# Kernel tuning notes

Measured on AMD Instinct MI355X. Metric: run time of the kernel, lower is better.

The kernel has to match this reference:

```python
import jax, jax.numpy as jnp
import numpy as np

B, N, D = 2, 1024, 1024
H, DH = 16, 64          # nhead, head_dim (D = H*DH)
FF = 4096               # dim_feedforward = 4*D
E = 8                   # num experts
EPS = 1e-5


def layer_norm(x, s, b):
    m = jnp.mean(x, -1, keepdims=True)
    v = jnp.mean((x - m) ** 2, -1, keepdims=True)
    return (x - m) * jax.lax.rsqrt(v + EPS) * s + b


def moe_gate(x, Wg):
    # top-1 gating: expert index + gate probability per token
    probs = jax.nn.softmax(x @ Wg, axis=-1)            # [B,N,E]
    idx = jnp.argmax(probs, axis=-1)                   # [B,N]
    gw = jnp.take_along_axis(probs, idx[..., None], -1)[..., 0]  # [B,N]
    return idx, gw


def moe_linear(x, W, b, idx, gw):
    # x:[B,N,Din], W:[E,Din,Dout], b:[E,Dout]; route each token to expert idx
    y = jnp.einsum('bnd,edh->bneh', x, W) + b          # [B,N,E,Dout]
    oh = jax.nn.one_hot(idx, E, dtype=x.dtype)         # [B,N,E]
    return jnp.einsum('bneh,bne->bnh', y, oh) * gw[..., None]


def setup_inputs() -> dict:
    key = jax.random.key(0)
    ks = jax.random.split(key, 8)
    g = lambda k, shape, sc: jax.random.normal(k, shape, jnp.float32) * sc
    inv_d = 1.0 / np.sqrt(D)
    return dict(
        src=g(ks[0], (B, N, D), 1.0),
        key_padding_mask=jnp.zeros((B, N), dtype=bool),
        Wg_attn=g(ks[1], (D, E), inv_d),
        Wqkv=g(ks[2], (E, D, 3 * D), inv_d), bqkv=jnp.zeros((E, 3 * D), jnp.float32),
        Wo=g(ks[3], (E, D, D), inv_d), bo=jnp.zeros((E, D), jnp.float32),
        Wg_ffn=g(ks[4], (D, E), inv_d),
        W1=g(ks[5], (E, D, FF), inv_d), b1=jnp.zeros((E, FF), jnp.float32),
        W2=g(ks[6], (E, FF, D), 1.0 / np.sqrt(FF)), b2=jnp.zeros((E, D), jnp.float32),
        ln1_s=jnp.ones((D,), jnp.float32), ln1_b=jnp.zeros((D,), jnp.float32),
        ln2_s=jnp.ones((D,), jnp.float32), ln2_b=jnp.zeros((D,), jnp.float32),
    )


def reference(src, key_padding_mask, Wg_attn, Wqkv, bqkv, Wo, bo,
              Wg_ffn, W1, b1, W2, b2, ln1_s, ln1_b, ln2_s, ln2_b):
    # attention mask: key_padding_mask.unsqueeze(1).unsqueeze(1) * -10000
    mask = jnp.where(key_padding_mask[:, None, None, :], -10000.0, 0.0).astype(src.dtype)

    # --- MoE self-attention (gate decided once, reused for qkv and dense) ---
    idx, gw = moe_gate(src, Wg_attn)
    qkv = moe_linear(src, Wqkv, bqkv, idx, gw)                 # [B,N,3D]
    q, k, v = jnp.split(qkv, 3, axis=-1)
    heads = lambda t: t.reshape(B, N, H, DH).transpose(0, 2, 1, 3)  # [B,H,N,DH]
    q, k, v = heads(q), heads(k), heads(v)
    scores = jnp.einsum('bhqd,bhkd->bhqk', q, k) / np.sqrt(DH) + mask
    probs = jax.nn.softmax(scores, axis=-1)
    ctx = jnp.einsum('bhqk,bhkd->bhqd', probs, v)
    ctx = ctx.transpose(0, 2, 1, 3).reshape(B, N, D)
    attn_out = moe_linear(ctx, Wo, bo, idx, gw)

    # post-norm residual
    x = layer_norm(src + attn_out, ln1_s, ln1_b)

    # --- MoE FFN (its own gate, shared across both linears) ---
    fidx, fgw = moe_gate(x, Wg_ffn)
    h = jax.nn.gelu(moe_linear(x, W1, b1, fidx, fgw))
    ffn = moe_linear(h, W2, b2, fidx, fgw)

    return layer_norm(x + ffn, ln2_s, ln2_b)
```

## Files before the change

### kernel.cpp

```cpp
#include <hip/hip_runtime.h>


#define B_   2
#define N_   1024
#define D_   1024
#define H_   16
#define DH_  64
#define FF_  4096
#define E_   8
#define NTOK 2048

typedef __attribute__((ext_vector_type(8))) short short8;
typedef __attribute__((ext_vector_type(8))) unsigned short ushort8;
typedef __attribute__((ext_vector_type(4))) unsigned short ushort4v;
typedef __attribute__((ext_vector_type(4))) float f32x4;
typedef __attribute__((ext_vector_type(2))) unsigned int uint32x2;

__device__ inline unsigned short f2bf(float f) {
  unsigned u = __float_as_uint(f);
  u += 0x7FFFu + ((u >> 16) & 1u);
  return (unsigned short)(u >> 16);
}

__device__ inline float gelu_tanh(float x) {
  float x3 = x * x * x;
  float t = tanhf(0.7978845608028654f * (x + 0.044715f * x3));
  return 0.5f * x * (1.0f + t);
}

__global__ __launch_bounds__(256) void gate_kernel(
    const float* __restrict__ X, const float* __restrict__ Wg,
    int* __restrict__ idx, float* __restrict__ gwv, int* __restrict__ cnt) {
  int t = blockIdx.x * 4 + (threadIdx.x >> 6);
  int lane = threadIdx.x & 63;
  const float* x = X + (size_t)t * D_;
  float acc[E_];
#pragma unroll
  for (int j = 0; j < E_; j++) acc[j] = 0.f;
#pragma unroll
  for (int i = 0; i < 16; i++) {
    int d = i * 64 + lane;
    float xv = x[d];
    const float4* w = (const float4*)(Wg + (size_t)d * E_);
    float4 w0 = w[0], w1 = w[1];
    acc[0] += xv * w0.x; acc[1] += xv * w0.y; acc[2] += xv * w0.z; acc[3] += xv * w0.w;
    acc[4] += xv * w1.x; acc[5] += xv * w1.y; acc[6] += xv * w1.z; acc[7] += xv * w1.w;
  }
#pragma unroll
  for (int o = 1; o < 64; o <<= 1) {
#pragma unroll
    for (int j = 0; j < E_; j++) acc[j] += __shfl_xor(acc[j], o, 64);
  }
  float m = acc[0]; int bi = 0;
#pragma unroll
  for (int j = 1; j < E_; j++) { if (acc[j] > m) { m = acc[j]; bi = j; } }
  float den = 0.f;
#pragma unroll
  for (int j = 0; j < E_; j++) den += expf(acc[j] - m);
  float gw = expf(acc[bi] - m) / den;
  if (lane == 0) { idx[t] = bi; gwv[t] = gw; atomicAdd(&cnt[bi], 1); }
}

__global__ __launch_bounds__(256) void route_kernel(
    const int* __restrict__ idx, const int* __restrict__ cnt,
    int* __restrict__ off, int* __restrict__ perm, int ntok) {
  __shared__ int loff[E_ + 1];
  __shared__ int lfill[E_];
  if (threadIdx.x == 0) {
    int s = 0;
    for (int e = 0; e < E_; e++) { loff[e] = s; s += cnt[e]; }
    loff[E_] = s;
  }
  if (threadIdx.x < E_) lfill[threadIdx.x] = 0;
  __syncthreads();
  for (int t = (int)threadIdx.x; t < ntok; t += 256) {
    int e = idx[t];
    int p = atomicAdd(&lfill[e], 1);
    perm[loff[e] + p] = t;
  }
  if (threadIdx.x < E_ + 1) off[threadIdx.x] = loff[threadIdx.x];
}

__global__ __launch_bounds__(256) void cast_bf16_kernel(
    const float* __restrict__ in, unsigned short* __restrict__ out) {
  size_t i = ((size_t)blockIdx.x * 256 + threadIdx.x) * 8;
  float4 v0 = *(const float4*)(in + i);
  float4 v1 = *(const float4*)(in + i + 4);
  ushort8 o;
  o[0] = f2bf(v0.x); o[1] = f2bf(v0.y); o[2] = f2bf(v0.z); o[3] = f2bf(v0.w);
  o[4] = f2bf(v1.x); o[5] = f2bf(v1.y); o[6] = f2bf(v1.z); o[7] = f2bf(v1.w);
  *(ushort8*)(out + i) = o;
}

template <int KS, int EPI>
__global__ __launch_bounds__(512, 2) void gemm_kernel(
    const unsigned short* __restrict__ A, int ldA,
    const float* __restrict__ W,
    const float* __restrict__ bias, const float* __restrict__ gwv,
    const int* __restrict__ perm, const int* __restrict__ off,
    void* __restrict__ outp, int K, int N) {
  __shared__ __align__(16) unsigned short As[256][32];
  __shared__ __align__(16) unsigned short Bs[128][40];
  __shared__ int toks[256];
  __shared__ float gws[256];

  int e = blockIdx.y;
  int base = off[e];
  int cnt = off[e + 1] - base;
  int mt = blockIdx.z / KS;
  int kc = blockIdx.z % KS;
  int m0 = mt * 256;
  if (m0 >= cnt) return;
  int rows_valid = min(256, cnt - m0);
  int tid = threadIdx.x;
  if (tid < 256) {
    int r = (tid < rows_valid) ? tid : (rows_valid - 1);
    int tk = perm[base + m0 + r];
    toks[tid] = tk;
    gws[tid] = gwv[tk];
  }
  int nb = blockIdx.x * 128;
  int lane = tid & 63, wave = tid >> 6;
  int wm = (wave & 3) * 64, wn = (wave >> 2) * 64;
  int lr = lane & 15, lg = lane >> 4;
  int aswz = (lg ^ ((lr >> 1) & 3)) << 3;
  int bswz = (lg ^ ((lr >> 2) & 3)) << 3;

  f32x4 acc[4][4];
#pragma unroll
  for (int m = 0; m < 4; m++)
#pragma unroll
    for (int n = 0; n < 4; n++) acc[m][n] = (f32x4){0.f, 0.f, 0.f, 0.f};

  bool isB = tid < 256;
  int c = tid & 31, rq = (tid >> 5) & 7;
  int k4 = rq * 4, n0 = c * 4;
  int arow = tid & 255;
  int as_ = (arow >> 1) & 3;

  int KL = K / KS, kbeg = kc * KL;
  int nt = KL / 32;
  __syncthreads();

  const unsigned short* abase = A + (size_t)toks[arow] * ldA;
  const float* wbase = W + ((size_t)e * K + k4) * N + nb + n0;

  ushort8 aR0, aR1, aR2, aR3;
  f32x4 bA0, bA1, bA2, bA3, bB0, bB1, bB2, bB3;

#define LOAD_A(KK) if (!isB) {                                            \
    const unsigned short* ap = abase + (KK);                              \
    aR0 = *(const ushort8*)ap;                                            \
    aR1 = *(const ushort8*)(ap + 8);                                      \
    aR2 = *(const ushort8*)(ap + 16);                                     \
    aR3 = *(const ushort8*)(ap + 24); }

#define LOAD_B(KK, R0, R1, R2, R3) if (isB) {                             \
    const float* wp = wbase + (size_t)(KK) * N;                           \
    R0 = *(const f32x4*)wp;                                               \
    R1 = *(const f32x4*)(wp + N);                                         \
    R2 = *(const f32x4*)(wp + 2 * N);                                     \
    R3 = *(const f32x4*)(wp + 3 * N); }

#define PUBLISH(R0, R1, R2, R3) {                                         \
    if (isB) {                                                            \
      _Pragma("unroll")                                                   \
      for (int j = 0; j < 4; j++) {                                       \
        int n = n0 + j;                                                   \
        int bb = (((k4 >> 3) ^ ((n >> 2) & 3)) << 3) | (k4 & 7);          \
        unsigned lo = (unsigned)f2bf(R0[j]) | ((unsigned)f2bf(R1[j]) << 16);\
        unsigned hi = (unsigned)f2bf(R2[j]) | ((unsigned)f2bf(R3[j]) << 16);\
        *(uint32x2*)&Bs[n][bb] = (uint32x2){lo, hi};                      \
      }                                                                   \
    } else {                                                              \
      *(ushort8*)&As[arow][(0 ^ as_) << 3] = aR0;                         \
      *(ushort8*)&As[arow][(1 ^ as_) << 3] = aR1;                         \
      *(ushort8*)&As[arow][(2 ^ as_) << 3] = aR2;                         \
      *(ushort8*)&As[arow][(3 ^ as_) << 3] = aR3;                         \
    } }

#define COMPUTE() {                                                       \
    short8 av[4], bv[4];                                                  \
    _Pragma("unroll")                                                     \
    for (int m = 0; m < 4; m++)                                           \
      av[m] = *(const short8*)&As[wm + m * 16 + lr][aswz];                \
    _Pragma("unroll")                                                     \
    for (int n = 0; n < 4; n++)                                           \
      bv[n] = *(const short8*)&Bs[wn + n * 16 + lr][bswz];                \
    __builtin_amdgcn_s_setprio(1);                                        \
    _Pragma("unroll")                                                     \
    for (int n = 0; n < 4; n++)                                           \
      _Pragma("unroll")                                                   \
      for (int m = 0; m < 4; m++)                                         \
        acc[m][n] = __builtin_amdgcn_mfma_f32_16x16x32_bf16(              \
            av[m], bv[n], acc[m][n], 0, 0, 0);                            \
    __builtin_amdgcn_s_setprio(0); }

  LOAD_A(kbeg);
  LOAD_B(kbeg, bA0, bA1, bA2, bA3);
  if (nt > 1) LOAD_B(kbeg + 32, bB0, bB1, bB2, bB3);

  for (int t = 0; t < nt; t += 2) {
    int k0 = kbeg + t * 32;
    PUBLISH(bA0, bA1, bA2, bA3);
    if (t + 1 < nt) LOAD_A(k0 + 32);
    if (t + 2 < nt) LOAD_B(k0 + 64, bA0, bA1, bA2, bA3);
    asm volatile("s_waitcnt lgkmcnt(0)" ::: "memory");
    __builtin_amdgcn_s_barrier();
    COMPUTE();
    __builtin_amdgcn_s_barrier();
    if (t + 1 < nt) {
      PUBLISH(bB0, bB1, bB2, bB3);
      if (t + 2 < nt) LOAD_A(k0 + 64);
      if (t + 3 < nt) LOAD_B(k0 + 96, bB0, bB1, bB2, bB3);
      asm volatile("s_waitcnt lgkmcnt(0)" ::: "memory");
      __builtin_amdgcn_s_barrier();
      COMPUTE();
      __builtin_amdgcn_s_barrier();
    }
  }
#undef LOAD_A
#undef LOAD_B
#undef PUBLISH
#undef COMPUTE

  if constexpr (EPI == 0) {
    float* pr = (float*)outp + (size_t)kc * ((size_t)NTOK * N);
#pragma unroll
    for (int n = 0; n < 4; n++) {
      int col = nb + wn + n * 16 + lr;
#pragma unroll
      for (int m = 0; m < 4; m++) {
#pragma unroll
        for (int reg = 0; reg < 4; reg++) {
          int r = wm + m * 16 + lg * 4 + reg;
          if (r < rows_valid)
            pr[(size_t)toks[r] * N + col] = acc[m][n][reg];
        }
      }
    }
  } else {
    unsigned short* po = (unsigned short*)outp;
    float bcol[4];
#pragma unroll
    for (int n = 0; n < 4; n++)
      bcol[n] = bias[(size_t)e * N + nb + wn + n * 16 + lr];
#pragma unroll
    for (int n = 0; n < 4; n++) {
      int col = nb + wn + n * 16 + lr;
#pragma unroll
      for (int m = 0; m < 4; m++) {
#pragma unroll
        for (int reg = 0; reg < 4; reg++) {
          int r = wm + m * 16 + lg * 4 + reg;
          if (r < rows_valid) {
            float v = (acc[m][n][reg] + bcol[n]) * gws[r];
            if constexpr (EPI == 2) v = gelu_tanh(v);
            po[(size_t)toks[r] * N + col] = f2bf(v);
          }
        }
      }
    }
  }
}

__global__ __launch_bounds__(256) void vtrans_kernel(
    const unsigned short* __restrict__ qkv, unsigned short* __restrict__ vT) {
  __shared__ __align__(16) unsigned short T[64][72];
  int bh = blockIdx.x;
  int b = bh >> 4, h = bh & 15;
  int tile = blockIdx.y;
  int tid = threadIdx.x;
  {
    int tk = tid >> 2, dof = (tid & 3) * 16;
    const unsigned short* p =
        qkv + ((size_t)(b * N_ + tile * 64 + tk)) * 3072 + 2048 + h * 64 + dof;
    *(ushort8*)&T[tk][dof] = *(const ushort8*)p;
    *(ushort8*)&T[tk][dof + 8] = *(const ushort8*)(p + 8);
  }
  __syncthreads();
  {
    int dh = tid >> 2, tof = (tid & 3) * 16;
    ushort8 o0, o1;
#pragma unroll
    for (int i = 0; i < 8; i++) o0[i] = T[tof + i][dh];
#pragma unroll
    for (int i = 0; i < 8; i++) o1[i] = T[tof + 8 + i][dh];
    unsigned short* q = vT + ((size_t)bh * 64 + dh) * N_ + tile * 64 + tof;
    *(ushort8*)q = o0;
    *(ushort8*)(q + 8) = o1;
  }
}

__global__ __launch_bounds__(256) void attn_kernel(
    const unsigned short* __restrict__ qkv, const unsigned short* __restrict__ vT,
    const unsigned char* __restrict__ kpm, unsigned short* __restrict__ ctx) {
  __shared__ __align__(16) unsigned short Qs[64][72];
  __shared__ __align__(16) unsigned short Ks[64][72];
  __shared__ __align__(16) unsigned short Vs[64][72];
  __shared__ __align__(16) unsigned short Ps[4][16][72];
  __shared__ float maskf[64];
  int qt = blockIdx.x, bh = blockIdx.y;
  int b = bh >> 4, h = bh & 15;
  int tid = threadIdx.x, lane = tid & 63, wave = tid >> 6;
  int lr = lane & 15, lg = lane >> 4;
  {
    int r = tid >> 2, dof = (tid & 3) * 16;
    const unsigned short* p = qkv + ((size_t)(b * N_ + qt * 64 + r)) * 3072 + h * 64 + dof;
    *(ushort8*)&Qs[r][dof] = *(const ushort8*)p;
    *(ushort8*)&Qs[r][dof + 8] = *(const ushort8*)(p + 8);
  }
  __syncthreads();
  short8 aq[2];
  aq[0] = *(const short8*)&Qs[wave * 16 + lr][lg * 8];
  aq[1] = *(const short8*)&Qs[wave * 16 + lr][32 + lg * 8];
  f32x4 O[4];
  float mrun[4], lrun[4];
#pragma unroll
  for (int r = 0; r < 4; r++) { mrun[r] = -1e30f; lrun[r] = 0.f; O[r] = (f32x4){0.f, 0.f, 0.f, 0.f}; }

  for (int kt = 0; kt < 16; kt++) {
    __syncthreads();
    {
      int r = tid >> 2, dof = (tid & 3) * 16;
      const unsigned short* p =
          qkv + ((size_t)(b * N_ + kt * 64 + r)) * 3072 + 1024 + h * 64 + dof;
      *(ushort8*)&Ks[r][dof] = *(const ushort8*)p;
      *(ushort8*)&Ks[r][dof + 8] = *(const ushort8*)(p + 8);
      const unsigned short* pv = vT + ((size_t)bh * 64 + r) * N_ + kt * 64 + dof;
      *(ushort8*)&Vs[r][dof] = *(const ushort8*)pv;
      *(ushort8*)&Vs[r][dof + 8] = *(const ushort8*)(pv + 8);
      if (tid < 64) maskf[tid] = kpm[b * N_ + kt * 64 + tid] ? -10000.f : 0.f;
    }
    __syncthreads();
    f32x4 S[4];
#pragma unroll
    for (int n = 0; n < 4; n++) {
      f32x4 s = (f32x4){0.f, 0.f, 0.f, 0.f};
#pragma unroll
      for (int ks = 0; ks < 2; ks++) {
        short8 bk = *(const short8*)&Ks[n * 16 + lr][ks * 32 + lg * 8];
        s = __builtin_amdgcn_mfma_f32_16x16x32_bf16(aq[ks], bk, s, 0, 0, 0);
      }
      float mv = maskf[n * 16 + lr];
#pragma unroll
      for (int r = 0; r < 4; r++) s[r] = s[r] * 0.125f + mv;
      S[n] = s;
    }
    float cur[4];
#pragma unroll
    for (int r = 0; r < 4; r++)
      cur[r] = fmaxf(fmaxf(S[0][r], S[1][r]), fmaxf(S[2][r], S[3][r]));
#pragma unroll
    for (int o = 1; o < 16; o <<= 1) {
#pragma unroll
      for (int r = 0; r < 4; r++) cur[r] = fmaxf(cur[r], __shfl_xor(cur[r], o, 64));
    }
    float alpha[4], rsum[4];
#pragma unroll
    for (int r = 0; r < 4; r++) {
      float mn = fmaxf(mrun[r], cur[r]);
      alpha[r] = expf(mrun[r] - mn);
      mrun[r] = mn;
      rsum[r] = 0.f;
    }
#pragma unroll
    for (int n = 0; n < 4; n++) {
#pragma unroll
      for (int r = 0; r < 4; r++) {
        S[n][r] = expf(S[n][r] - mrun[r]);
        rsum[r] += S[n][r];
      }
    }
#pragma unroll
    for (int o = 1; o < 16; o <<= 1) {
#pragma unroll
      for (int r = 0; r < 4; r++) rsum[r] += __shfl_xor(rsum[r], o, 64);
    }
#pragma unroll
    for (int r = 0; r < 4; r++) lrun[r] = lrun[r] * alpha[r] + rsum[r];
#pragma unroll
    for (int d = 0; d < 4; d++)
#pragma unroll
      for (int r = 0; r < 4; r++) O[d][r] *= alpha[r];
#pragma unroll
    for (int n = 0; n < 4; n++)
#pragma unroll
      for (int r = 0; r < 4; r++) Ps[wave][lg * 4 + r][n * 16 + lr] = f2bf(S[n][r]);
    short8 pf[2];
    pf[0] = *(const short8*)&Ps[wave][lr][lg * 8];
    pf[1] = *(const short8*)&Ps[wave][lr][32 + lg * 8];
#pragma unroll
    for (int d = 0; d < 4; d++) {
#pragma unroll
      for (int ks = 0; ks < 2; ks++) {
        short8 bv = *(const short8*)&Vs[d * 16 + lr][ks * 32 + lg * 8];
        O[d] = __builtin_amdgcn_mfma_f32_16x16x32_bf16(pf[ks], bv, O[d], 0, 0, 0);
      }
    }
  }
#pragma unroll
  for (int r = 0; r < 4; r++) lrun[r] = 1.f / lrun[r];
#pragma unroll
  for (int d = 0; d < 4; d++) {
#pragma unroll
    for (int r = 0; r < 4; r++) {
      int q = qt * 64 + wave * 16 + lg * 4 + r;
      int dh = d * 16 + lr;
      ctx[((size_t)(b * N_ + q)) * D_ + h * DH_ + dh] = f2bf(O[d][r] * lrun[r]);
    }
  }
}

template <int KS, bool WBF>
__global__ __launch_bounds__(256) void ln_reduce_kernel(
    const float* __restrict__ res, const float* __restrict__ part,
    const float* __restrict__ bias, const float* __restrict__ gwv,
    const int* __restrict__ idx,
    const float* __restrict__ S, const float* __restrict__ Bi,
    float* __restrict__ O, unsigned short* __restrict__ Obf) {
  int t = blockIdx.x, tid = threadIdx.x;
  int e = idx[t];
  float gw = gwv[t];
  const float* p = part + (size_t)t * D_ + tid * 4;
  float4 a = *(const float4*)p;
#pragma unroll
  for (int k = 1; k < KS; k++) {
    float4 q = *(const float4*)(p + (size_t)k * NTOK * D_);
    a.x += q.x; a.y += q.y; a.z += q.z; a.w += q.w;
  }
  float4 bv4 = *(const float4*)(bias + (size_t)e * D_ + tid * 4);
  float4 vr = ((const float4*)(res + (size_t)t * D_))[tid];
  float4 v;
  v.x = vr.x + (a.x + bv4.x) * gw;
  v.y = vr.y + (a.y + bv4.y) * gw;
  v.z = vr.z + (a.z + bv4.z) * gw;
  v.w = vr.w + (a.w + bv4.w) * gw;
  float s = v.x + v.y + v.z + v.w;
  float sq = v.x * v.x + v.y * v.y + v.z * v.z + v.w * v.w;
#pragma unroll
  for (int o = 1; o < 64; o <<= 1) {
    s += __shfl_xor(s, o, 64);
    sq += __shfl_xor(sq, o, 64);
  }
  __shared__ float ss[4], ssq[4];
  int wave = tid >> 6, lane = tid & 63;
  if (lane == 0) { ss[wave] = s; ssq[wave] = sq; }
  __syncthreads();
  float ts = ss[0] + ss[1] + ss[2] + ss[3];
  float tsq = ssq[0] + ssq[1] + ssq[2] + ssq[3];
  float mean = ts * (1.f / D_);
  float var = tsq * (1.f / D_) - mean * mean;
  float rs = rsqrtf(var + 1e-5f);
  float4 sv = ((const float4*)S)[tid];
  float4 bi = ((const float4*)Bi)[tid];
  float4 o;
  o.x = (v.x - mean) * rs * sv.x + bi.x;
  o.y = (v.y - mean) * rs * sv.y + bi.y;
  o.z = (v.z - mean) * rs * sv.z + bi.z;
  o.w = (v.w - mean) * rs * sv.w + bi.w;
  ((float4*)(O + (size_t)t * D_))[tid] = o;
  if constexpr (WBF) {
    ushort4v ob;
    ob[0] = f2bf(o.x); ob[1] = f2bf(o.y); ob[2] = f2bf(o.z); ob[3] = f2bf(o.w);
    *(ushort4v*)(Obf + (size_t)t * D_ + tid * 4) = ob;
  }
}

extern "C" void kernel_launch(void* const* d_in, const int* in_sizes, int n_in,
                              void* d_out, int out_size, void* d_ws, size_t ws_size,
                              hipStream_t stream) {
  (void)in_sizes; (void)n_in; (void)out_size; (void)ws_size;
  const float* src     = (const float*)d_in[0];
  const unsigned char* kpm = (const unsigned char*)d_in[1];
  const float* Wg_attn = (const float*)d_in[2];
  const float* Wqkv    = (const float*)d_in[3];
  const float* bqkv    = (const float*)d_in[4];
  const float* Wo      = (const float*)d_in[5];
  const float* bo      = (const float*)d_in[6];
  const float* Wg_ffn  = (const float*)d_in[7];
  const float* W1      = (const float*)d_in[8];
  const float* b1      = (const float*)d_in[9];
  const float* W2      = (const float*)d_in[10];
  const float* b2      = (const float*)d_in[11];
  const float* ln1_s   = (const float*)d_in[12];
  const float* ln1_b   = (const float*)d_in[13];
  const float* ln2_s   = (const float*)d_in[14];
  const float* ln2_b   = (const float*)d_in[15];
  float* out = (float*)d_out;

  char* ws = (char*)d_ws;
  size_t o = 0;
  auto alloc = [&](size_t bytes) -> void* {
    void* p = ws + o;
    o += (bytes + 255) & ~(size_t)255;
    return p;
  };
  int* meta = (int*)alloc(256);
  int* cnt1 = meta;
  int* off1 = meta + 8;
  int* cnt2 = meta + 17;
  int* off2 = meta + 25;
  int* idx1 = (int*)alloc(NTOK * 4);
  float* gw1 = (float*)alloc(NTOK * 4);
  int* perm1 = (int*)alloc(NTOK * 4);
  int* idx2 = (int*)alloc(NTOK * 4);
  float* gw2 = (float*)alloc(NTOK * 4);
  int* perm2 = (int*)alloc(NTOK * 4);
  unsigned short* qkvb = (unsigned short*)alloc((size_t)NTOK * 3072 * 2);
  unsigned short* vT = (unsigned short*)alloc((size_t)32 * 64 * N_ * 2);
  unsigned short* hbuf = qkvb;
  unsigned short* ctx = (unsigned short*)alloc((size_t)NTOK * D_ * 2);
  unsigned short* src_bf = ctx;
  unsigned short* x_bf = ctx;
  float* x = (float*)alloc((size_t)NTOK * D_ * 4);
  float* part = (float*)alloc((size_t)2 * NTOK * D_ * 4);

  hipMemsetAsync(meta, 0, 256, stream);

  cast_bf16_kernel<<<1024, 256, 0, stream>>>(src, src_bf);
  gate_kernel<<<512, 256, 0, stream>>>(src, Wg_attn, idx1, gw1, cnt1);
  route_kernel<<<1, 256, 0, stream>>>(idx1, cnt1, off1, perm1, NTOK);
  gemm_kernel<1, 1><<<dim3(3072 / 128, 8, 8), 512, 0, stream>>>(
      src_bf, 1024, Wqkv, bqkv, gw1, perm1, off1, qkvb, 1024, 3072);
  vtrans_kernel<<<dim3(32, 16), 256, 0, stream>>>(qkvb, vT);
  attn_kernel<<<dim3(16, 32), 256, 0, stream>>>(qkvb, vT, kpm, ctx);
  gemm_kernel<2, 0><<<dim3(1024 / 128, 8, 16), 512, 0, stream>>>(
      ctx, 1024, Wo, bo, gw1, perm1, off1, part, 1024, 1024);
  ln_reduce_kernel<2, true><<<NTOK, 256, 0, stream>>>(
      src, part, bo, gw1, idx1, ln1_s, ln1_b, x, x_bf);

  gate_kernel<<<512, 256, 0, stream>>>(x, Wg_ffn, idx2, gw2, cnt2);
  route_kernel<<<1, 256, 0, stream>>>(idx2, cnt2, off2, perm2, NTOK);
  gemm_kernel<1, 2><<<dim3(4096 / 128, 8, 8), 512, 0, stream>>>(
      x_bf, 1024, W1, b1, gw2, perm2, off2, hbuf, 1024, 4096);
  gemm_kernel<2, 0><<<dim3(1024 / 128, 8, 16), 512, 0, stream>>>(
      hbuf, 4096, W2, b2, gw2, perm2, off2, part, 4096, 1024);
  ln_reduce_kernel<2, false><<<NTOK, 256, 0, stream>>>(
      x, part, b2, gw2, idx2, ln2_s, ln2_b, out, (unsigned short*)nullptr);
}
```

Measured before the change: 653.5 us.

## Halve GEMM N-tile, double split-K, and interleave experts in block order

The grouped MoE GEMM tile is narrowed from 256x128 to 256x64 output columns, with B staging and accumulators shrunk to match. Split-K for the Wo and W2 GEMMs goes from 2 to 4, and the partial buffer and reduce kernel are widened accordingly. Block IDs are remapped so the expert index varies fastest, spreading uneven expert loads across CUs. The aim is more blocks and better balance in exchange for more A reloads per output, more partial-sum traffic, and less MFMA work per wave.

```diff
diff --git a/kernel.cpp b/kernel.cpp
--- a/kernel.cpp
+++ b/kernel.cpp
@@ -14,7 +14,6 @@
 typedef __attribute__((ext_vector_type(8))) unsigned short ushort8;
 typedef __attribute__((ext_vector_type(4))) unsigned short ushort4v;
 typedef __attribute__((ext_vector_type(4))) float f32x4;
-typedef __attribute__((ext_vector_type(2))) unsigned int uint32x2;
 
 __device__ inline unsigned short f2bf(float f) {
   unsigned u = __float_as_uint(f);
@@ -100,15 +99,21 @@
     const int* __restrict__ perm, const int* __restrict__ off,
     void* __restrict__ outp, int K, int N) {
   __shared__ __align__(16) unsigned short As[256][32];
-  __shared__ __align__(16) unsigned short Bs[128][40];
+  __shared__ __align__(16) unsigned short Bs[64][40];
   __shared__ int toks[256];
   __shared__ float gws[256];
 
-  int e = blockIdx.y;
+  unsigned gx = gridDim.x;
+  unsigned id = blockIdx.x + gx * (blockIdx.y + 8u * blockIdx.z);
+  int e = id & 7;
+  unsigned r_ = id >> 3;
+  int nbi = r_ % gx;
+  int zz = r_ / gx;
+  int mt = zz / KS;
+  int kc = zz % KS;
+
   int base = off[e];
   int cnt = off[e + 1] - base;
-  int mt = blockIdx.z / KS;
-  int kc = blockIdx.z % KS;
   int m0 = mt * 256;
   if (m0 >= cnt) return;
   int rows_valid = min(256, cnt - m0);
@@ -119,22 +124,22 @@
     toks[tid] = tk;
     gws[tid] = gwv[tk];
   }
-  int nb = blockIdx.x * 128;
+  int nbase = nbi * 64;
   int lane = tid & 63, wave = tid >> 6;
-  int wm = (wave & 3) * 64, wn = (wave >> 2) * 64;
+  int wm = (wave & 3) * 64, wn = (wave >> 2) * 32;
   int lr = lane & 15, lg = lane >> 4;
   int aswz = (lg ^ ((lr >> 1) & 3)) << 3;
   int bswz = (lg ^ ((lr >> 2) & 3)) << 3;
 
-  f32x4 acc[4][4];
+  f32x4 acc[4][2];
 #pragma unroll
   for (int m = 0; m < 4; m++)
 #pragma unroll
-    for (int n = 0; n < 4; n++) acc[m][n] = (f32x4){0.f, 0.f, 0.f, 0.f};
+    for (int n = 0; n < 2; n++) acc[m][n] = (f32x4){0.f, 0.f, 0.f, 0.f};
 
   bool isB = tid < 256;
-  int c = tid & 31, rq = (tid >> 5) & 7;
-  int k4 = rq * 4, n0 = c * 4;
+  int c = tid & 15, rq = (tid >> 4) & 15;
+  int k2 = rq * 2, n0 = c * 4;
   int arow = tid & 255;
   int as_ = (arow >> 1) & 3;
 
@@ -143,10 +148,10 @@
   __syncthreads();
 
   const unsigned short* abase = A + (size_t)toks[arow] * ldA;
-  const float* wbase = W + ((size_t)e * K + k4) * N + nb + n0;
+  const float* wbase = W + ((size_t)e * K + k2) * N + nbase + n0;
 
   ushort8 aR0, aR1, aR2, aR3;
-  f32x4 bA0, bA1, bA2, bA3, bB0, bB1, bB2, bB3;
+  f32x4 bA0, bA1, bB0, bB1;
 
 #define LOAD_A(KK) if (!isB) {                                            \
     const unsigned short* ap = abase + (KK);                              \
@@ -155,22 +160,19 @@
     aR2 = *(const ushort8*)(ap + 16);                                     \
     aR3 = *(const ushort8*)(ap + 24); }
 
-#define LOAD_B(KK, R0, R1, R2, R3) if (isB) {                             \
+#define LOAD_B(KK, R0, R1) if (isB) {                                     \
     const float* wp = wbase + (size_t)(KK) * N;                           \
     R0 = *(const f32x4*)wp;                                               \
-    R1 = *(const f32x4*)(wp + N);                                         \
-    R2 = *(const f32x4*)(wp + 2 * N);                                     \
-    R3 = *(const f32x4*)(wp + 3 * N); }
-
-#define PUBLISH(R0, R1, R2, R3) {                                         \
+    R1 = *(const f32x4*)(wp + N); }
+
+#define PUBLISH(R0, R1) {                                                 \
     if (isB) {                                                            \
       _Pragma("unroll")                                                   \
       for (int j = 0; j < 4; j++) {                                       \
         int n = n0 + j;                                                   \
-        int bb = (((k4 >> 3) ^ ((n >> 2) & 3)) << 3) | (k4 & 7);          \
-        unsigned lo = (unsigned)f2bf(R0[j]) | ((unsigned)f2bf(R1[j]) << 16);\
-        unsigned hi = (unsigned)f2bf(R2[j]) | ((unsigned)f2bf(R3[j]) << 16);\
-        *(uint32x2*)&Bs[n][bb] = (uint32x2){lo, hi};                      \
+        int bb = (((k2 >> 3) ^ ((n >> 2) & 3)) << 3) | (k2 & 7);          \
+        unsigned v = (unsigned)f2bf(R0[j]) | ((unsigned)f2bf(R1[j]) << 16);\
+        *(unsigned*)&Bs[n][bb] = v;                                       \
       }                                                                   \
     } else {                                                              \
       *(ushort8*)&As[arow][(0 ^ as_) << 3] = aR0;                         \
@@ -180,16 +182,16 @@
     } }
 
 #define COMPUTE() {                                                       \
-    short8 av[4], bv[4];                                                  \
+    short8 av[4], bv[2];                                                  \
     _Pragma("unroll")                                                     \
     for (int m = 0; m < 4; m++)                                           \
       av[m] = *(const short8*)&As[wm + m * 16 + lr][aswz];                \
     _Pragma("unroll")                                                     \
-    for (int n = 0; n < 4; n++)                                           \
+    for (int n = 0; n < 2; n++)                                           \
       bv[n] = *(const short8*)&Bs[wn + n * 16 + lr][bswz];                \
     __builtin_amdgcn_s_setprio(1);                                        \
     _Pragma("unroll")                                                     \
-    for (int n = 0; n < 4; n++)                                           \
+    for (int n = 0; n < 2; n++)                                           \
       _Pragma("unroll")                                                   \
       for (int m = 0; m < 4; m++)                                         \
         acc[m][n] = __builtin_amdgcn_mfma_f32_16x16x32_bf16(              \
@@ -197,22 +199,22 @@
     __builtin_amdgcn_s_setprio(0); }
 
   LOAD_A(kbeg);
-  LOAD_B(kbeg, bA0, bA1, bA2, bA3);
-  if (nt > 1) LOAD_B(kbeg + 32, bB0, bB1, bB2, bB3);
+  LOAD_B(kbeg, bA0, bA1);
+  if (nt > 1) LOAD_B(kbeg + 32, bB0, bB1);
 
   for (int t = 0; t < nt; t += 2) {
     int k0 = kbeg + t * 32;
-    PUBLISH(bA0, bA1, bA2, bA3);
+    PUBLISH(bA0, bA1);
     if (t + 1 < nt) LOAD_A(k0 + 32);
-    if (t + 2 < nt) LOAD_B(k0 + 64, bA0, bA1, bA2, bA3);
+    if (t + 2 < nt) LOAD_B(k0 + 64, bA0, bA1);
     asm volatile("s_waitcnt lgkmcnt(0)" ::: "memory");
     __builtin_amdgcn_s_barrier();
     COMPUTE();
     __builtin_amdgcn_s_barrier();
     if (t + 1 < nt) {
-      PUBLISH(bB0, bB1, bB2, bB3);
+      PUBLISH(bB0, bB1);
       if (t + 2 < nt) LOAD_A(k0 + 64);
-      if (t + 3 < nt) LOAD_B(k0 + 96, bB0, bB1, bB2, bB3);
+      if (t + 3 < nt) LOAD_B(k0 + 96, bB0, bB1);
       asm volatile("s_waitcnt lgkmcnt(0)" ::: "memory");
       __builtin_amdgcn_s_barrier();
       COMPUTE();
@@ -227,8 +229,8 @@
   if constexpr (EPI == 0) {
     float* pr = (float*)outp + (size_t)kc * ((size_t)NTOK * N);
 #pragma unroll
-    for (int n = 0; n < 4; n++) {
-      int col = nb + wn + n * 16 + lr;
+    for (int n = 0; n < 2; n++) {
+      int col = nbase + wn + n * 16 + lr;
 #pragma unroll
       for (int m = 0; m < 4; m++) {
 #pragma unroll
@@ -241,13 +243,13 @@
     }
   } else {
     unsigned short* po = (unsigned short*)outp;
-    float bcol[4];
-#pragma unroll
-    for (int n = 0; n < 4; n++)
-      bcol[n] = bias[(size_t)e * N + nb + wn + n * 16 + lr];
-#pragma unroll
-    for (int n = 0; n < 4; n++) {
-      int col = nb + wn + n * 16 + lr;
+    float bcol[2];
+#pragma unroll
+    for (int n = 0; n < 2; n++)
+      bcol[n] = bias[(size_t)e * N + nbase + wn + n * 16 + lr];
+#pragma unroll
+    for (int n = 0; n < 2; n++) {
+      int col = nbase + wn + n * 16 + lr;
 #pragma unroll
       for (int m = 0; m < 4; m++) {
 #pragma unroll
@@ -514,28 +516,28 @@
   unsigned short* src_bf = ctx;
   unsigned short* x_bf = ctx;
   float* x = (float*)alloc((size_t)NTOK * D_ * 4);
-  float* part = (float*)alloc((size_t)2 * NTOK * D_ * 4);
+  float* part = (float*)alloc((size_t)4 * NTOK * D_ * 4);
 
   hipMemsetAsync(meta, 0, 256, stream);
 
   cast_bf16_kernel<<<1024, 256, 0, stream>>>(src, src_bf);
   gate_kernel<<<512, 256, 0, stream>>>(src, Wg_attn, idx1, gw1, cnt1);
   route_kernel<<<1, 256, 0, stream>>>(idx1, cnt1, off1, perm1, NTOK);
-  gemm_kernel<1, 1><<<dim3(3072 / 128, 8, 8), 512, 0, stream>>>(
+  gemm_kernel<1, 1><<<dim3(3072 / 64, 8, 8), 512, 0, stream>>>(
       src_bf, 1024, Wqkv, bqkv, gw1, perm1, off1, qkvb, 1024, 3072);
   vtrans_kernel<<<dim3(32, 16), 256, 0, stream>>>(qkvb, vT);
   attn_kernel<<<dim3(16, 32), 256, 0, stream>>>(qkvb, vT, kpm, ctx);
-  gemm_kernel<2, 0><<<dim3(1024 / 128, 8, 16), 512, 0, stream>>>(
+  gemm_kernel<4, 0><<<dim3(1024 / 64, 8, 32), 512, 0, stream>>>(
       ctx, 1024, Wo, bo, gw1, perm1, off1, part, 1024, 1024);
-  ln_reduce_kernel<2, true><<<NTOK, 256, 0, stream>>>(
+  ln_reduce_kernel<4, true><<<NTOK, 256, 0, stream>>>(
       src, part, bo, gw1, idx1, ln1_s, ln1_b, x, x_bf);
 
   gate_kernel<<<512, 256, 0, stream>>>(x, Wg_ffn, idx2, gw2, cnt2);
   route_kernel<<<1, 256, 0, stream>>>(idx2, cnt2, off2, perm2, NTOK);
-  gemm_kernel<1, 2><<<dim3(4096 / 128, 8, 8), 512, 0, stream>>>(
+  gemm_kernel<1, 2><<<dim3(4096 / 64, 8, 8), 512, 0, stream>>>(
       x_bf, 1024, W1, b1, gw2, perm2, off2, hbuf, 1024, 4096);
-  gemm_kernel<2, 0><<<dim3(1024 / 128, 8, 16), 512, 0, stream>>>(
+  gemm_kernel<4, 0><<<dim3(1024 / 64, 8, 32), 512, 0, stream>>>(
       hbuf, 4096, W2, b2, gw2, perm2, off2, part, 4096, 1024);
-  ln_reduce_kernel<2, false><<<NTOK, 256, 0, stream>>>(
+  ln_reduce_kernel<4, false><<<NTOK, 256, 0, stream>>>(
       x, part, b2, gw2, idx2, ln2_s, ln2_b, out, (unsigned short*)nullptr);
 }
```

New measurement: 713.1 us. 1.09x slower.
